# Kernel tuning notes

Hardware: AMD Instinct MI355X
Metric: run time of the kernel (lower is better)

The kernel has to match this reference:

```python
import jax, jax.numpy as jnp
import numpy as np

N_NODES = 50000
N_GRAPHS = 512
EPS = 1e-5


def _ln(x, g, b):
    mu = jnp.mean(x, axis=-1, keepdims=True)
    var = jnp.var(x, axis=-1, keepdims=True)
    return (x - mu) * jax.lax.rsqrt(var + EPS) * g + b


def _sage(x, src, dst, wl, wr, bl):
    # mean-aggregate neighbor features: messages x[src] -> dst
    s = jax.ops.segment_sum(x[src], dst, num_segments=N_NODES)
    cnt = jax.ops.segment_sum(jnp.ones((src.shape[0],), x.dtype), dst, num_segments=N_NODES)
    agg = s / jnp.maximum(cnt, 1.0)[:, None]
    # PyG SAGEConv: lin_l(agg) + lin_r(x), bias only on lin_l
    return agg @ wl + bl + x @ wr


def setup_inputs() -> dict:
    key = jax.random.key(0)
    ks = jax.random.split(key, 16)
    C, H, NC, E = 128, 128, 2, 800000
    inp = {
        'x': jax.random.normal(ks[0], (N_NODES, C), jnp.float32),
        'edge_index': jax.random.randint(ks[1], (2, E), 0, N_NODES, jnp.int32),
        'batch': jnp.sort(jax.random.randint(ks[2], (N_NODES,), 0, N_GRAPHS, jnp.int32)),
    }
    def w(k, shape):
        return jax.random.normal(k, shape, jnp.float32) * 0.05
    inp.update({
        'w1l': w(ks[3], (C, H)), 'w1r': w(ks[4], (C, H)), 'b1': jnp.zeros((H,), jnp.float32),
        'g1': jnp.ones((H,), jnp.float32), 'be1': jnp.zeros((H,), jnp.float32),
        'w2l': w(ks[5], (H, H)), 'w2r': w(ks[6], (H, H)), 'b2': jnp.zeros((H,), jnp.float32),
        'g2': jnp.ones((H,), jnp.float32), 'be2': jnp.zeros((H,), jnp.float32),
        'w3l': w(ks[7], (H, H)), 'w3r': w(ks[8], (H, H)), 'b3': jnp.zeros((H,), jnp.float32),
        'g3': jnp.ones((H,), jnp.float32), 'be3': jnp.zeros((H,), jnp.float32),
        'wc': w(ks[9], (H, NC)), 'bc': jnp.zeros((NC,), jnp.float32),
    })
    return inp


def reference(x, edge_index, batch, w1l, w1r, b1, g1, be1, w2l, w2r, b2, g2, be2,
              w3l, w3r, b3, g3, be3, wc, bc):
    src, dst = edge_index[0], edge_index[1]
    # eval mode: dropout is identity
    h1 = _ln(jax.nn.relu(_sage(x, src, dst, w1l, w1r, b1)), g1, be1)
    h2 = _ln(jax.nn.relu(_sage(h1, src, dst, w2l, w2r, b2)) + h1, g2, be2)
    h3 = _ln(h2 + jax.nn.relu(_sage(h2, src, dst, w3l, w3r, b3)), g3, be3)
    # global mean pool over graphs
    s = jax.ops.segment_sum(h3, batch, num_segments=N_GRAPHS)
    cnt = jax.ops.segment_sum(jnp.ones((h3.shape[0],), h3.dtype), batch, num_segments=N_GRAPHS)
    avg = s / jnp.maximum(cnt, 1.0)[:, None]
    out = avg @ wc + bc
    return (out, h3, avg)
```

## Files before the change

kernel.cpp:

```cpp
#include <hip/hip_runtime.h>

#define NND 50000
#define NE  800000
#define CF  128
#define NGR 512
#define DCAP 64

typedef __bf16 bf16;
typedef __bf16 bf16x2 __attribute__((ext_vector_type(2)));
typedef __bf16 bf16x4 __attribute__((ext_vector_type(4)));
typedef __bf16 bf16x8 __attribute__((ext_vector_type(8)));
typedef float  f32x4  __attribute__((ext_vector_type(4)));

__global__ __launch_bounds__(256) void zero_k(int4* __restrict__ p) {
  p[blockIdx.x * 256 + threadIdx.x] = int4{0, 0, 0, 0};
}

__global__ __launch_bounds__(256) void convfill_k(const float* __restrict__ x,
                                                  bf16* __restrict__ xb,
                                                  const float* __restrict__ w1l, const float* __restrict__ w1r,
                                                  const float* __restrict__ w2l, const float* __restrict__ w2r,
                                                  const float* __restrict__ w3l, const float* __restrict__ w3r,
                                                  bf16* __restrict__ wb,
                                                  const int* __restrict__ batch,
                                                  int* __restrict__ gs,
                                                  const int* __restrict__ src,
                                                  const int* __restrict__ dst,
                                                  int* __restrict__ cnt,
                                                  unsigned short* __restrict__ csr) {
  if (blockIdx.x < 6250) {
    int t = blockIdx.x * 256 + threadIdx.x;
    {
      f32x4 v = ((const f32x4*)x)[t];
      bf16x4 o;
      o[0] = (bf16)v[0]; o[1] = (bf16)v[1]; o[2] = (bf16)v[2]; o[3] = (bf16)v[3];
      ((bf16x4*)xb)[t] = o;
    }
    if (t < 49152) {
      int m = t >> 13, w2 = t & 8191;
      const float* sp = (m == 0) ? w1l : (m == 1) ? w1r : (m == 2) ? w2l
                      : (m == 3) ? w2r : (m == 4) ? w3l : w3r;
      int e0 = w2 * 2;
      int k = e0 >> 7, n = e0 & 127;
      float2 v = *(const float2*)(sp + e0);
      bf16* wm = wb + m * 16384;
      wm[n * 128       + ((((k >> 3) ^ (n       & 15)) << 3)) + (k & 7)] = (bf16)v.x;
      wm[(n + 1) * 128 + ((((k >> 3) ^ ((n + 1) & 15)) << 3)) + (k & 7)] = (bf16)v.y;
    }
    if (t < NND) {
      int b = batch[t];
      if (t == 0) {
        for (int g = 0; g <= b; g++) gs[g] = 0;
      } else {
        int pb = batch[t - 1];
        for (int g = pb + 1; g <= b; g++) gs[g] = t;
      }
      if (t == NND - 1) {
        for (int g = b + 1; g <= NGR; g++) gs[g] = NND;
      }
    }
  } else {
    int bb = blockIdx.x - 6250;
    int r  = bb & 7;
    int lo = r * 6250, hi = lo + 6250;
    int ebase = (bb >> 3) * 2048;
#pragma unroll
    for (int h = 0; h < 2; h++) {
      int e = ebase + h * 1024 + threadIdx.x * 4;
      if (e < NE) {
        int4 d4 = *(const int4*)(dst + e);
        int4 s4 = *(const int4*)(src + e);
        int dd[4] = {d4.x, d4.y, d4.z, d4.w};
        int ss[4] = {s4.x, s4.y, s4.z, s4.w};
#pragma unroll
        for (int u = 0; u < 4; u++) {
          int d = dd[u];
          if (d >= lo && d < hi) {
            int p = atomicAdd(&cnt[d], 1);
            if (p < DCAP) csr[d * DCAP + p] = (unsigned short)ss[u];
          }
        }
      }
    }
  }
}

__global__ __launch_bounds__(256) void agg_k(const bf16* __restrict__ xin,
                                             const int* __restrict__ cnt,
                                             const unsigned short* __restrict__ csr,
                                             bf16* __restrict__ aggout) {
  int b    = blockIdx.x;
  int half = b & 1;
  int node = (b >> 1) * 4 + (threadIdx.x >> 6);
  int lane = threadIdx.x & 63;
  int sub  = lane >> 3;
  int c8   = half * 64 + (lane & 7) * 8;
  int deg  = min(cnt[node], DCAP);
  int ebase = node * DCAP;
  float a[8] = {};
  {
    int s[4]; float m[4]; bf16x8 v[4];
#pragma unroll
    for (int u = 0; u < 2; u++) {
      int i = u * 8 + sub;
      s[u] = csr[ebase + ((i < deg) ? i : 0)];
      m[u] = (i < deg) ? 1.f : 0.f;
    }
#pragma unroll
    for (int u = 0; u < 2; u++) v[u] = *(const bf16x8*)(xin + s[u] * 128 + c8);
    if (deg > 16) {
#pragma unroll
      for (int u = 2; u < 4; u++) {
        int i = u * 8 + sub;
        s[u] = csr[ebase + ((i < deg) ? i : 0)];
        m[u] = (i < deg) ? 1.f : 0.f;
      }
#pragma unroll
      for (int u = 2; u < 4; u++) v[u] = *(const bf16x8*)(xin + s[u] * 128 + c8);
    }
#pragma unroll
    for (int u = 0; u < 2; u++)
#pragma unroll
      for (int j = 0; j < 8; j++) a[j] += m[u] * (float)v[u][j];
    if (deg > 16) {
#pragma unroll
      for (int u = 2; u < 4; u++)
#pragma unroll
        for (int j = 0; j < 8; j++) a[j] += m[u] * (float)v[u][j];
    }
  }
  for (int e = 32; e < deg; e += 8) {
    int i = e + sub;
    int s = csr[ebase + ((i < deg) ? i : 0)];
    float m = (i < deg) ? 1.f : 0.f;
    bf16x8 v = *(const bf16x8*)(xin + s * 128 + c8);
#pragma unroll
    for (int j = 0; j < 8; j++) a[j] += m * (float)v[j];
  }
#pragma unroll
  for (int j = 0; j < 8; j++) {
    a[j] += __shfl_xor(a[j], 8);
    a[j] += __shfl_xor(a[j], 16);
    a[j] += __shfl_xor(a[j], 32);
  }
  if (sub == 0) {
    float inv = 1.0f / fmaxf((float)deg, 1.0f);
    bf16x8 o;
#pragma unroll
    for (int j = 0; j < 8; j++) o[j] = (bf16)(a[j] * inv);
    *(bf16x8*)(aggout + node * 128 + c8) = o;
  }
}

template <typename TO>
__global__ __launch_bounds__(256, 4) void gemm_k(
    const bf16* __restrict__ aggp, const bf16* __restrict__ prev,
    const bf16* __restrict__ wswz,
    const float* __restrict__ bias, const float* __restrict__ gamma,
    const float* __restrict__ beta, TO* __restrict__ outp, int addres) {
  __shared__ bf16 bt[16384];
  int tid = threadIdx.x;
  int lane = tid & 63;
  int wave = tid >> 6;
  int q = lane >> 4, r = lane & 15;
  int wrow = blockIdx.x * 64 + wave * 16;
  int arow = min(wrow + r, NND - 1);

  {
    const bf16x8* g = (const bf16x8*)wswz;
#pragma unroll
    for (int i = 0; i < 8; i++)
      ((bf16x8*)bt)[tid + i * 256] = g[tid + i * 256];
  }
  bf16x8 af0[4], af1[4];
  {
    const bf16* a0 = aggp + arow * 128 + q * 8;
    const bf16* a1 = prev + arow * 128 + q * 8;
#pragma unroll
    for (int kk = 0; kk < 4; kk++) af0[kk] = *(const bf16x8*)(a0 + kk * 32);
#pragma unroll
    for (int kk = 0; kk < 4; kk++) af1[kk] = *(const bf16x8*)(a1 + kk * 32);
  }
  __syncthreads();

  f32x4 acc[8] = {};
#pragma unroll
  for (int kk = 0; kk < 4; kk++) {
#pragma unroll
    for (int t = 0; t < 8; t++) {
      int n = t * 16 + r;
      bf16x8 bfrag = *(const bf16x8*)&bt[n * 128 + (((kk * 4 + q) ^ (n & 15)) << 3)];
      acc[t] = __builtin_amdgcn_mfma_f32_16x16x32_bf16(af0[kk], bfrag, acc[t], 0, 0, 0);
    }
  }
  __syncthreads();
  {
    const bf16x8* g = (const bf16x8*)(wswz + 16384);
#pragma unroll
    for (int i = 0; i < 8; i++)
      ((bf16x8*)bt)[tid + i * 256] = g[tid + i * 256];
  }
  __syncthreads();
#pragma unroll
  for (int kk = 0; kk < 4; kk++) {
#pragma unroll
    for (int t = 0; t < 8; t++) {
      int n = t * 16 + r;
      bf16x8 bfrag = *(const bf16x8*)&bt[n * 128 + (((kk * 4 + q) ^ (n & 15)) << 3)];
      acc[t] = __builtin_amdgcn_mfma_f32_16x16x32_bf16(af1[kk], bfrag, acc[t], 0, 0, 0);
    }
  }

  float biasf[8], gf[8], bef[8];
#pragma unroll
  for (int t = 0; t < 8; t++) {
    int c = t * 16 + r;
    biasf[t] = bias[c];
    gf[t]    = gamma[c];
    bef[t]   = beta[c];
  }

#pragma unroll
  for (int reg = 0; reg < 4; reg++) {
    int row = wrow + q * 4 + reg;
    int rr  = (row < NND) ? row : (NND - 1);
    const bf16* prow = prev + rr * 128;
    float vals[8];
    float s = 0.f, s2 = 0.f;
#pragma unroll
    for (int t = 0; t < 8; t++) {
      float v = acc[t][reg] + biasf[t];
      v = fmaxf(v, 0.f);
      if (addres) v += (float)prow[t * 16 + r];
      vals[t] = v;
      s += v;
      s2 += v * v;
    }
#pragma unroll
    for (int m = 1; m < 16; m <<= 1) {
      s  += __shfl_xor(s, m);
      s2 += __shfl_xor(s2, m);
    }
    float mean = s * (1.f / 128.f);
    float var  = fmaxf(s2 * (1.f / 128.f) - mean * mean, 0.f);
    float rstd = rsqrtf(var + 1e-5f);
    if (row < NND) {
      TO* orow = outp + row * 128;
#pragma unroll
      for (int t = 0; t < 8; t++)
        orow[t * 16 + r] = (TO)((vals[t] - mean) * rstd * gf[t] + bef[t]);
    }
  }
}

__global__ __launch_bounds__(256) void poolhead_k(
    const float* __restrict__ h3, const int* __restrict__ gs,
    const float* __restrict__ wc, const float* __restrict__ bc,
    float* __restrict__ outv, float* __restrict__ avgv) {
  int g = blockIdx.x;
  int s = gs[g], epos = gs[g + 1];
  int tid = threadIdx.x;
  int wave = tid >> 6, lane = tid & 63;
  float a0 = 0.f, a1 = 0.f;
  for (int row = s + wave; row < epos; row += 4) {
    float2 v = *(const float2*)(h3 + row * 128 + 2 * lane);
    a0 += v.x; a1 += v.y;
  }
  __shared__ float red[4][128];
  red[wave][2 * lane]     = a0;
  red[wave][2 * lane + 1] = a1;
  __syncthreads();
  __shared__ float sp[4];
  if (tid < 128) {
    float t4  = red[0][tid] + red[1][tid] + red[2][tid] + red[3][tid];
    float inv = 1.f / fmaxf((float)(epos - s), 1.f);
    float avg = t4 * inv;
    avgv[g * 128 + tid] = avg;
    float p0 = avg * wc[tid * 2 + 0];
    float p1 = avg * wc[tid * 2 + 1];
#pragma unroll
    for (int m = 1; m < 64; m <<= 1) {
      p0 += __shfl_xor(p0, m);
      p1 += __shfl_xor(p1, m);
    }
    if ((tid & 63) == 0) {
      sp[(tid >> 6) * 2]     = p0;
      sp[(tid >> 6) * 2 + 1] = p1;
    }
  }
  __syncthreads();
  if (tid == 0) {
    outv[g * 2 + 0] = sp[0] + sp[2] + bc[0];
    outv[g * 2 + 1] = sp[1] + sp[3] + bc[1];
  }
}

extern "C" void kernel_launch(void* const* d_in, const int* in_sizes, int n_in,
                              void* d_out, int out_size, void* d_ws, size_t ws_size,
                              hipStream_t stream) {
  const float* x   = (const float*)d_in[0];
  const int* ei    = (const int*)d_in[1];
  const int* batch = (const int*)d_in[2];
  const float* w1l = (const float*)d_in[3],  *w1r = (const float*)d_in[4];
  const float* b1  = (const float*)d_in[5],  *g1  = (const float*)d_in[6],  *be1 = (const float*)d_in[7];
  const float* w2l = (const float*)d_in[8],  *w2r = (const float*)d_in[9];
  const float* b2  = (const float*)d_in[10], *g2  = (const float*)d_in[11], *be2 = (const float*)d_in[12];
  const float* w3l = (const float*)d_in[13], *w3r = (const float*)d_in[14];
  const float* b3  = (const float*)d_in[15], *g3  = (const float*)d_in[16], *be3 = (const float*)d_in[17];
  const float* wc  = (const float*)d_in[18], *bc  = (const float*)d_in[19];
  const int* srcv = ei;
  const int* dstv = ei + NE;

  char* base = (char*)d_ws;
  int*            cnt  = (int*)(base + 0);
  int*            gs   = (int*)(base + 200704);
  bf16*           wb   = (bf16*)(base + 204800);
  unsigned short* csr  = (unsigned short*)(base + 401408);
  bf16*           agg  = (bf16*)(base + 6801408);
  bf16*           h1   = (bf16*)(base + 19601408);
  bf16*           h2xb = (bf16*)(base + 32401408);

  float* outv = (float*)d_out;
  float* h3   = outv + 1024;
  float* avgv = outv + 1024 + NND * CF;

  zero_k<<<49, 256, 0, stream>>>((int4*)base);
  convfill_k<<<9378, 256, 0, stream>>>(x, h2xb, w1l, w1r, w2l, w2r, w3l, w3r, wb,
                                       batch, gs, srcv, dstv, cnt, csr);

  agg_k<<<25000, 256, 0, stream>>>(h2xb, cnt, csr, agg);
  gemm_k<bf16><<<782, 256, 0, stream>>>(agg, h2xb, wb,           b1, g1, be1, h1, 0);
  agg_k<<<25000, 256, 0, stream>>>(h1, cnt, csr, agg);
  gemm_k<bf16><<<782, 256, 0, stream>>>(agg, h1, wb + 2 * 16384, b2, g2, be2, h2xb, 1);
  agg_k<<<25000, 256, 0, stream>>>(h2xb, cnt, csr, agg);
  gemm_k<float><<<782, 256, 0, stream>>>(agg, h2xb, wb + 4 * 16384, b3, g3, be3, h3, 1);
  poolhead_k<<<NGR, 256, 0, stream>>>(h3, gs, wc, bc, outv, avgv);
}
```

Measured before the change: 308.4 us.

## Fuse neighbor mean-aggregation into the SAGE GEMM kernel

Removes the separate per-layer aggregation kernel and gathers neighbor features directly inside the GEMM kernel. Each thread accumulates 32 channels of its row over the CSR neighbor list and turns the mean into MFMA A-fragments. This drops the round trip of the aggregated buffer through global memory and three kernel launches. The cost is far less parallelism for the latency-bound gather: 782 blocks with a serial per-thread edge loop instead of 25000 blocks, plus wave imbalance across rows of different degree.

```diff
diff --git a/kernel.cpp b/kernel.cpp
--- a/kernel.cpp
+++ b/kernel.cpp
@@ -37,10 +37,10 @@
       ((bf16x4*)xb)[t] = o;
     }
     if (t < 49152) {
-      int m = t >> 13, w2 = t & 8191;
+      int m = t >> 13, w2i = t & 8191;
       const float* sp = (m == 0) ? w1l : (m == 1) ? w1r : (m == 2) ? w2l
                       : (m == 3) ? w2r : (m == 4) ? w3l : w3r;
-      int e0 = w2 * 2;
+      int e0 = w2i * 2;
       int k = e0 >> 7, n = e0 & 127;
       float2 v = *(const float2*)(sp + e0);
       bf16* wm = wb + m * 16384;
@@ -85,76 +85,10 @@
   }
 }
 
-__global__ __launch_bounds__(256) void agg_k(const bf16* __restrict__ xin,
-                                             const int* __restrict__ cnt,
-                                             const unsigned short* __restrict__ csr,
-                                             bf16* __restrict__ aggout) {
-  int b    = blockIdx.x;
-  int half = b & 1;
-  int node = (b >> 1) * 4 + (threadIdx.x >> 6);
-  int lane = threadIdx.x & 63;
-  int sub  = lane >> 3;
-  int c8   = half * 64 + (lane & 7) * 8;
-  int deg  = min(cnt[node], DCAP);
-  int ebase = node * DCAP;
-  float a[8] = {};
-  {
-    int s[4]; float m[4]; bf16x8 v[4];
-#pragma unroll
-    for (int u = 0; u < 2; u++) {
-      int i = u * 8 + sub;
-      s[u] = csr[ebase + ((i < deg) ? i : 0)];
-      m[u] = (i < deg) ? 1.f : 0.f;
-    }
-#pragma unroll
-    for (int u = 0; u < 2; u++) v[u] = *(const bf16x8*)(xin + s[u] * 128 + c8);
-    if (deg > 16) {
-#pragma unroll
-      for (int u = 2; u < 4; u++) {
-        int i = u * 8 + sub;
-        s[u] = csr[ebase + ((i < deg) ? i : 0)];
-        m[u] = (i < deg) ? 1.f : 0.f;
-      }
-#pragma unroll
-      for (int u = 2; u < 4; u++) v[u] = *(const bf16x8*)(xin + s[u] * 128 + c8);
-    }
-#pragma unroll
-    for (int u = 0; u < 2; u++)
-#pragma unroll
-      for (int j = 0; j < 8; j++) a[j] += m[u] * (float)v[u][j];
-    if (deg > 16) {
-#pragma unroll
-      for (int u = 2; u < 4; u++)
-#pragma unroll
-        for (int j = 0; j < 8; j++) a[j] += m[u] * (float)v[u][j];
-    }
-  }
-  for (int e = 32; e < deg; e += 8) {
-    int i = e + sub;
-    int s = csr[ebase + ((i < deg) ? i : 0)];
-    float m = (i < deg) ? 1.f : 0.f;
-    bf16x8 v = *(const bf16x8*)(xin + s * 128 + c8);
-#pragma unroll
-    for (int j = 0; j < 8; j++) a[j] += m * (float)v[j];
-  }
-#pragma unroll
-  for (int j = 0; j < 8; j++) {
-    a[j] += __shfl_xor(a[j], 8);
-    a[j] += __shfl_xor(a[j], 16);
-    a[j] += __shfl_xor(a[j], 32);
-  }
-  if (sub == 0) {
-    float inv = 1.0f / fmaxf((float)deg, 1.0f);
-    bf16x8 o;
-#pragma unroll
-    for (int j = 0; j < 8; j++) o[j] = (bf16)(a[j] * inv);
-    *(bf16x8*)(aggout + node * 128 + c8) = o;
-  }
-}
-
 template <typename TO>
-__global__ __launch_bounds__(256, 4) void gemm_k(
-    const bf16* __restrict__ aggp, const bf16* __restrict__ prev,
+__global__ __launch_bounds__(256, 5) void aggemm_k(
+    const bf16* __restrict__ xp,
+    const int* __restrict__ cnt, const unsigned short* __restrict__ csr,
     const bf16* __restrict__ wswz,
     const float* __restrict__ bias, const float* __restrict__ gamma,
     const float* __restrict__ beta, TO* __restrict__ outp, int addres) {
@@ -172,14 +106,53 @@
     for (int i = 0; i < 8; i++)
       ((bf16x8*)bt)[tid + i * 256] = g[tid + i * 256];
   }
-  bf16x8 af0[4], af1[4];
+  bf16x8 af1[4];
   {
-    const bf16* a0 = aggp + arow * 128 + q * 8;
-    const bf16* a1 = prev + arow * 128 + q * 8;
-#pragma unroll
-    for (int kk = 0; kk < 4; kk++) af0[kk] = *(const bf16x8*)(a0 + kk * 32);
+    const bf16* a1 = xp + arow * 128 + q * 8;
 #pragma unroll
     for (int kk = 0; kk < 4; kk++) af1[kk] = *(const bf16x8*)(a1 + kk * 32);
+  }
+
+  int deg = min(cnt[arow], DCAP);
+  const unsigned short* cp = csr + arow * DCAP;
+  const bf16* xq = xp + q * 8;
+  float fa[4][8] = {};
+  int e = 0;
+  for (; e + 2 <= deg; e += 2) {
+    ushort2 ss = *(const ushort2*)(cp + e);
+    const bf16* p0 = xq + (int)ss.x * 128;
+    const bf16* p1 = xq + (int)ss.y * 128;
+    bf16x8 v0[4], v1[4];
+#pragma unroll
+    for (int kk = 0; kk < 4; kk++) {
+      v0[kk] = *(const bf16x8*)(p0 + kk * 32);
+      v1[kk] = *(const bf16x8*)(p1 + kk * 32);
+    }
+#pragma unroll
+    for (int kk = 0; kk < 4; kk++)
+#pragma unroll
+      for (int j = 0; j < 8; j++)
+        fa[kk][j] += (float)v0[kk][j] + (float)v1[kk][j];
+  }
+  if (e < deg) {
+    const bf16* p0 = xq + (int)cp[e] * 128;
+#pragma unroll
+    for (int kk = 0; kk < 4; kk++) {
+      bf16x8 vt = *(const bf16x8*)(p0 + kk * 32);
+#pragma unroll
+      for (int j = 0; j < 8; j++) fa[kk][j] += (float)vt[j];
+    }
+  }
+  bf16x8 af0[4];
+  {
+    float inv = 1.0f / fmaxf((float)deg, 1.0f);
+#pragma unroll
+    for (int kk = 0; kk < 4; kk++) {
+      bf16x8 o;
+#pragma unroll
+      for (int j = 0; j < 8; j++) o[j] = (bf16)(fa[kk][j] * inv);
+      af0[kk] = o;
+    }
   }
   __syncthreads();
 
@@ -224,7 +197,7 @@
   for (int reg = 0; reg < 4; reg++) {
     int row = wrow + q * 4 + reg;
     int rr  = (row < NND) ? row : (NND - 1);
-    const bf16* prow = prev + rr * 128;
+    const bf16* prow = xp + rr * 128;
     float vals[8];
     float s = 0.f, s2 = 0.f;
 #pragma unroll
@@ -316,7 +289,6 @@
   int*            gs   = (int*)(base + 200704);
   bf16*           wb   = (bf16*)(base + 204800);
   unsigned short* csr  = (unsigned short*)(base + 401408);
-  bf16*           agg  = (bf16*)(base + 6801408);
   bf16*           h1   = (bf16*)(base + 19601408);
   bf16*           h2xb = (bf16*)(base + 32401408);
 
@@ -328,11 +300,8 @@
   convfill_k<<<9378, 256, 0, stream>>>(x, h2xb, w1l, w1r, w2l, w2r, w3l, w3r, wb,
                                        batch, gs, srcv, dstv, cnt, csr);
 
-  agg_k<<<25000, 256, 0, stream>>>(h2xb, cnt, csr, agg);
-  gemm_k<bf16><<<782, 256, 0, stream>>>(agg, h2xb, wb,           b1, g1, be1, h1, 0);
-  agg_k<<<25000, 256, 0, stream>>>(h1, cnt, csr, agg);
-  gemm_k<bf16><<<782, 256, 0, stream>>>(agg, h1, wb + 2 * 16384, b2, g2, be2, h2xb, 1);
-  agg_k<<<25000, 256, 0, stream>>>(h2xb, cnt, csr, agg);
-  gemm_k<float><<<782, 256, 0, stream>>>(agg, h2xb, wb + 4 * 16384, b3, g3, be3, h3, 1);
+  aggemm_k<bf16><<<782, 256, 0, stream>>>(h2xb, cnt, csr, wb,           b1, g1, be1, h1, 0);
+  aggemm_k<bf16><<<782, 256, 0, stream>>>(h1, cnt, csr, wb + 2 * 16384, b2, g2, be2, h2xb, 1);
+  aggemm_k<float><<<782, 256, 0, stream>>>(h2xb, cnt, csr, wb + 4 * 16384, b3, g3, be3, h3, 1);
   poolhead_k<<<NGR, 256, 0, stream>>>(h3, gs, wc, bc, outv, avgv);
 }
```

After: 325.0 us. +5.4%, slower.
